# Performance work log

Measured on AMD Instinct MI355X. Metric: run time of the kernel, lower is better.

The kernel has to match this reference:

```python
import jax, jax.numpy as jnp
import numpy as np

NORMALIZE_EPS = 1e-5
INV_DELTA = 15.0
DIST_NORM_PREV = 0.5  # init value of _dist_norm_prev buffer (eval-mode constant)
SKIP_OFFSET = 2


def _l2_normalize(v, axis, eps=NORMALIZE_EPS):
    # matches torch F.normalize: v / max(||v||, eps)
    n = jnp.sqrt(jnp.sum(v * v, axis=axis, keepdims=True))
    return v / jnp.maximum(n, eps)


def setup_inputs() -> dict:
    key = jax.random.key(0)
    k1, k2 = jax.random.split(key)
    x = jax.random.normal(k1, (128, 197, 768), dtype=jnp.float32)
    emb = jnp.clip(jax.random.normal(k2, (4096, 768), dtype=jnp.float32), 0.0, None)
    emb = _l2_normalize(emb, axis=1)
    return {"x": x, "embedding": emb}


def reference(x, embedding):
    # drop CLS token -> [N, L, C] with L = H*W
    x = x[:, 1:, :]
    N, L, C = x.shape
    height = width = int(np.sqrt(L))
    # assign_words: L2-normalize tokens, cosine distance to codebook
    xn = _l2_normalize(x, axis=2)
    dist = -jnp.einsum("nlc,kc->nlk", xn, embedding)  # [N, L, K]
    inv_delta = INV_DELTA / DIST_NORM_PREV
    codes = jax.nn.softmax(-inv_delta * dist, axis=2)  # [N, L, K]
    # compute_bow: drop border tokens, mean-pool, L1-normalize
    grid = jnp.arange(height * width).reshape(height, width)
    keep = grid[SKIP_OFFSET:-SKIP_OFFSET, SKIP_OFFSET:-SKIP_OFFSET].reshape(-1)
    bow = jnp.mean(codes[:, keep, :], axis=1)  # [N, K]
    bow = bow / jnp.maximum(jnp.sum(jnp.abs(bow), axis=1, keepdims=True), NORMALIZE_EPS)
    return bow, codes
```

## Files before the change

### kernel.cpp

```cpp
#include <hip/hip_runtime.h>


typedef unsigned short ushort_t;
typedef short short8 __attribute__((ext_vector_type(8)));
typedef float float4_ __attribute__((ext_vector_type(4)));

#define M_ROWS 25088
#define N_COLS 4096
#define K_DIM  768
#define BM 128
#define BN 128
#define BK 32

__device__ __forceinline__ unsigned short f2bf_rne(float f) {
  unsigned u = __float_as_uint(f);
  unsigned r = u + 0x7fffu + ((u >> 16) & 1u);
  return (unsigned short)(r >> 16);
}
__device__ __forceinline__ float bf2f(unsigned short h) {
  return __uint_as_float(((unsigned)h) << 16);
}

__device__ __forceinline__ void gload16(const void* g, void* l) {
  __builtin_amdgcn_global_load_lds(
      (__attribute__((address_space(1))) void*)g,
      (__attribute__((address_space(3))) void*)l, 16, 0, 0);
}

__global__ void split_emb_kernel(const float* __restrict__ emb,
                                 ushort_t* __restrict__ Bh,
                                 ushort_t* __restrict__ Bl) {
  int t = blockIdx.x * 256 + threadIdx.x;
  float f = emb[t];
  unsigned short h = f2bf_rne(f);
  Bh[t] = h;
  Bl[t] = f2bf_rne(f - bf2f(h));
}

__global__ void norm_split_x_kernel(const float* __restrict__ x,
                                    ushort_t* __restrict__ Ah,
                                    ushort_t* __restrict__ Al) {
  int m = blockIdx.x;
  int n = m / 196;
  int l = m - n * 196;
  size_t src = ((size_t)n * 197 + 1 + l) * 768;
  int t = threadIdx.x;

  float v0 = x[src + t];
  float v1 = x[src + t + 256];
  float v2 = x[src + t + 512];
  float s = v0 * v0 + v1 * v1 + v2 * v2;
  #pragma unroll
  for (int off = 32; off; off >>= 1) s += __shfl_xor(s, off, 64);
  __shared__ float ws4[4];
  if ((t & 63) == 0) ws4[t >> 6] = s;
  __syncthreads();
  s = ws4[0] + ws4[1] + ws4[2] + ws4[3];
  float scale = 1.0f / fmaxf(sqrtf(s), 1e-5f);

  size_t dst = (size_t)m * 768;
  float f[3] = {v0 * scale, v1 * scale, v2 * scale};
  int idx[3] = {t, t + 256, t + 512};
  #pragma unroll
  for (int i = 0; i < 3; i++) {
    unsigned short h = f2bf_rne(f[i]);
    Ah[dst + idx[i]] = h;
    Al[dst + idx[i]] = f2bf_rne(f[i] - bf2f(h));
  }
}

__global__ __launch_bounds__(256, 2)
void gemm_exp_kernel(const ushort_t* __restrict__ Ah, const ushort_t* __restrict__ Al,
                     const ushort_t* __restrict__ Bh, const ushort_t* __restrict__ Bl,
                     float* __restrict__ codes, float* __restrict__ rowsum) {
  __shared__ __attribute__((aligned(16))) ushort_t sAh[BM * BK];
  __shared__ __attribute__((aligned(16))) ushort_t sAl[BM * BK];
  __shared__ __attribute__((aligned(16))) ushort_t sBh[BM * BK];
  __shared__ __attribute__((aligned(16))) ushort_t sBl[BM * BK];
  __shared__ float rs[BM];

  const int t = threadIdx.x;
  const int w = t >> 6;
  const int lane = t & 63;
  const int row0 = blockIdx.x * BM;
  const int col0 = blockIdx.y * BN;

  if (t < BM) rs[t] = 0.f;

  float4_ acc[4][4];
  #pragma unroll
  for (int i = 0; i < 4; i++)
    #pragma unroll
    for (int j = 0; j < 4; j++) acc[i][j] = (float4_){0.f, 0.f, 0.f, 0.f};

  const int r0 = t >> 2;
  const int c0 = (((t & 3) ^ ((r0 >> 1) & 3))) * 8;
  const ushort_t* gA = Ah + (size_t)(row0 + r0) * K_DIM + c0;
  const ushort_t* gAl_ = Al + (size_t)(row0 + r0) * K_DIM + c0;
  const ushort_t* gB = Bh + (size_t)(col0 + r0) * K_DIM + c0;
  const ushort_t* gBl_ = Bl + (size_t)(col0 + r0) * K_DIM + c0;
  const int half = 64 * K_DIM;
  const int ldsw = w * 512;

  const int rl = (w >> 1) * 64;
  const int cl = (w & 1) * 64;
  const int lq = lane >> 4;
  const int li = lane & 15;
  const int fsw = (li >> 1) & 3;
  const int abase = (rl + li) * BK + (lq ^ fsw) * 8;
  const int bbase = (cl + li) * BK + (lq ^ fsw) * 8;

  for (int kk = 0; kk < K_DIM; kk += BK) {
    __syncthreads();
    gload16(gA + kk,           sAh + ldsw);
    gload16(gA + kk + half,    sAh + 2048 + ldsw);
    gload16(gAl_ + kk,         sAl + ldsw);
    gload16(gAl_ + kk + half,  sAl + 2048 + ldsw);
    gload16(gB + kk,           sBh + ldsw);
    gload16(gB + kk + half,    sBh + 2048 + ldsw);
    gload16(gBl_ + kk,         sBl + ldsw);
    gload16(gBl_ + kk + half,  sBl + 2048 + ldsw);
    __syncthreads();

    short8 ah[4], al[4], bh[4], bl[4];
    #pragma unroll
    for (int i = 0; i < 4; i++) {
      ah[i] = *(const short8*)(sAh + abase + i * 16 * BK);
      al[i] = *(const short8*)(sAl + abase + i * 16 * BK);
      bh[i] = *(const short8*)(sBh + bbase + i * 16 * BK);
      bl[i] = *(const short8*)(sBl + bbase + i * 16 * BK);
    }
    #pragma unroll
    for (int i = 0; i < 4; i++)
      #pragma unroll
      for (int j = 0; j < 4; j++) {
        acc[i][j] = __builtin_amdgcn_mfma_f32_16x16x32_bf16(ah[i], bh[j], acc[i][j], 0, 0, 0);
        acc[i][j] = __builtin_amdgcn_mfma_f32_16x16x32_bf16(ah[i], bl[j], acc[i][j], 0, 0, 0);
        acc[i][j] = __builtin_amdgcn_mfma_f32_16x16x32_bf16(al[i], bh[j], acc[i][j], 0, 0, 0);
      }
  }

  float rsum[4][4];
  #pragma unroll
  for (int i = 0; i < 4; i++)
    #pragma unroll
    for (int r = 0; r < 4; r++) rsum[i][r] = 0.f;

  #pragma unroll
  for (int i = 0; i < 4; i++)
    #pragma unroll
    for (int j = 0; j < 4; j++)
      #pragma unroll
      for (int r = 0; r < 4; r++) {
        float e = __expf(30.0f * acc[i][j][r]);
        size_t row = (size_t)(row0 + rl + i * 16 + lq * 4 + r);
        size_t col = (size_t)(col0 + cl + j * 16 + li);
        codes[row * N_COLS + col] = e;
        rsum[i][r] += e;
      }

  #pragma unroll
  for (int i = 0; i < 4; i++)
    #pragma unroll
    for (int r = 0; r < 4; r++) {
      float v = rsum[i][r];
      v += __shfl_xor(v, 1, 64);
      v += __shfl_xor(v, 2, 64);
      v += __shfl_xor(v, 4, 64);
      v += __shfl_xor(v, 8, 64);
      if (li == 0) atomicAdd(&rs[rl + i * 16 + lq * 4 + r], v);
    }
  __syncthreads();
  if (t < BM) atomicAdd(&rowsum[row0 + t], rs[t]);
}

__global__ __launch_bounds__(256)
void rescale_bow_kernel(float* __restrict__ codes,
                        const float* __restrict__ rowsum,
                        float* __restrict__ bow_un,
                        float* __restrict__ bow_l1) {
  const int n = blockIdx.x >> 2;
  const int t = threadIdx.x;
  const int k4 = (blockIdx.x & 3) * 256 + t;

  __shared__ float inv[196];
  __shared__ float keep[196];
  if (t < 196) {
    inv[t] = 1.0f / rowsum[n * 196 + t];
    int rr = t / 14;
    int cc = t - rr * 14;
    keep[t] = (rr >= 2 && rr <= 11 && cc >= 2 && cc <= 11) ? 0.01f : 0.0f;
  }
  __syncthreads();

  float4_* base = (float4_*)(codes + (size_t)n * 196 * N_COLS) + k4;
  float4_ acc = {0.f, 0.f, 0.f, 0.f};
  #pragma unroll 2
  for (int l = 0; l < 196; l++) {
    float4_ v = base[(size_t)l * 1024];
    float iv = inv[l];
    v.x *= iv; v.y *= iv; v.z *= iv; v.w *= iv;
    base[(size_t)l * 1024] = v;
    float kf = keep[l];
    acc.x += kf * v.x; acc.y += kf * v.y;
    acc.z += kf * v.z; acc.w += kf * v.w;
  }

  ((float4_*)(bow_un + (size_t)n * N_COLS))[k4] = acc;

  float s = fabsf(acc.x) + fabsf(acc.y) + fabsf(acc.z) + fabsf(acc.w);
  #pragma unroll
  for (int off = 32; off; off >>= 1) s += __shfl_xor(s, off, 64);
  __shared__ float wsum[4];
  if ((t & 63) == 0) wsum[t >> 6] = s;
  __syncthreads();
  if (t == 0) atomicAdd(&bow_l1[n], wsum[0] + wsum[1] + wsum[2] + wsum[3]);
}

__global__ void bow_norm_kernel(const float* __restrict__ bow_un,
                                const float* __restrict__ bow_l1,
                                float* __restrict__ bow_out) {
  int t = blockIdx.x * 256 + threadIdx.x;
  int n = t >> 12;
  bow_out[t] = bow_un[t] / fmaxf(bow_l1[n], 1e-5f);
}

extern "C" void kernel_launch(void* const* d_in, const int* in_sizes, int n_in,
                              void* d_out, int out_size, void* d_ws, size_t ws_size,
                              hipStream_t stream) {
  const float* x = (const float*)d_in[0];
  const float* emb = (const float*)d_in[1];
  float* bow_out = (float*)d_out;
  float* codes = (float*)d_out + 524288;

  char* ws = (char*)d_ws;
  ushort_t* Ah = (ushort_t*)(ws + 0);
  ushort_t* Al = (ushort_t*)(ws + 38535168);
  ushort_t* Bh = (ushort_t*)(ws + 77070336);
  ushort_t* Bl = (ushort_t*)(ws + 83361792);
  float* rowsum = (float*)(ws + 89653248);
  float* bow_un = (float*)(ws + 89753600);
  float* bow_l1 = (float*)(ws + 91850752);

  hipMemsetAsync(rowsum, 0, 25088 * 4, stream);
  hipMemsetAsync(bow_l1, 0, 128 * 4, stream);

  split_emb_kernel<<<12288, 256, 0, stream>>>(emb, Bh, Bl);
  norm_split_x_kernel<<<25088, 256, 0, stream>>>(x, Ah, Al);

  dim3 ggrid(M_ROWS / BM, N_COLS / BN);
  gemm_exp_kernel<<<ggrid, 256, 0, stream>>>(Ah, Al, Bh, Bl, codes, rowsum);

  rescale_bow_kernel<<<512, 256, 0, stream>>>(codes, rowsum, bow_un, bow_l1);
  bow_norm_kernel<<<2048, 256, 0, stream>>>(bow_un, bow_l1, bow_out);
}
```

Measured before the change: 1.084 ms.

## Split rescale over token groups with atomics, fuse L1 norm, raise GEMM occupancy

The rescale/bow kernel now splits the 196 tokens of each image into 4 groups of 49, launching 2048 blocks instead of 512. Each block unrolls loads 7 at a time for more memory-level parallelism and accumulates partial bow sums with float atomics into a zeroed buffer. The L1 norm reduction moves into a per-image bow_norm kernel. Separately, the GEMM's launch bounds are raised to 4 waves-per-SIMD occupancy, which may force register spills given its large accumulator and fragment arrays.

```diff
diff --git a/kernel.cpp b/kernel.cpp
--- a/kernel.cpp
+++ b/kernel.cpp
@@ -69,7 +69,7 @@
   }
 }
 
-__global__ __launch_bounds__(256, 2)
+__global__ __launch_bounds__(256, 4)
 void gemm_exp_kernel(const ushort_t* __restrict__ Ah, const ushort_t* __restrict__ Al,
                      const ushort_t* __restrict__ Bh, const ushort_t* __restrict__ Bl,
                      float* __restrict__ codes, float* __restrict__ rowsum) {
@@ -177,52 +177,79 @@
 __global__ __launch_bounds__(256)
 void rescale_bow_kernel(float* __restrict__ codes,
                         const float* __restrict__ rowsum,
-                        float* __restrict__ bow_un,
-                        float* __restrict__ bow_l1) {
-  const int n = blockIdx.x >> 2;
+                        float* __restrict__ bow_un) {
+  const int bid = blockIdx.x;
+  const int n = bid >> 4;
+  const int g = (bid >> 2) & 3;
+  const int chunk = bid & 3;
   const int t = threadIdx.x;
-  const int k4 = (blockIdx.x & 3) * 256 + t;
-
-  __shared__ float inv[196];
-  __shared__ float keep[196];
-  if (t < 196) {
-    inv[t] = 1.0f / rowsum[n * 196 + t];
-    int rr = t / 14;
-    int cc = t - rr * 14;
+  const int k4 = chunk * 256 + t;
+  const int l0 = g * 49;
+
+  __shared__ float inv[49];
+  __shared__ float keep[49];
+  if (t < 49) {
+    int l = l0 + t;
+    inv[t] = 1.0f / rowsum[n * 196 + l];
+    int rr = l / 14;
+    int cc = l - rr * 14;
     keep[t] = (rr >= 2 && rr <= 11 && cc >= 2 && cc <= 11) ? 0.01f : 0.0f;
   }
   __syncthreads();
 
-  float4_* base = (float4_*)(codes + (size_t)n * 196 * N_COLS) + k4;
+  float4_* base = (float4_*)(codes + (size_t)n * 196 * N_COLS)
+                  + (size_t)l0 * 1024 + k4;
   float4_ acc = {0.f, 0.f, 0.f, 0.f};
-  #pragma unroll 2
-  for (int l = 0; l < 196; l++) {
-    float4_ v = base[(size_t)l * 1024];
-    float iv = inv[l];
-    v.x *= iv; v.y *= iv; v.z *= iv; v.w *= iv;
-    base[(size_t)l * 1024] = v;
-    float kf = keep[l];
-    acc.x += kf * v.x; acc.y += kf * v.y;
-    acc.z += kf * v.z; acc.w += kf * v.w;
-  }
-
-  ((float4_*)(bow_un + (size_t)n * N_COLS))[k4] = acc;
-
-  float s = fabsf(acc.x) + fabsf(acc.y) + fabsf(acc.z) + fabsf(acc.w);
+  #pragma unroll
+  for (int c = 0; c < 7; c++) {
+    float4_ v[7];
+    #pragma unroll
+    for (int u = 0; u < 7; u++) v[u] = base[(size_t)(c * 7 + u) * 1024];
+    #pragma unroll
+    for (int u = 0; u < 7; u++) {
+      int l = c * 7 + u;
+      float iv = inv[l];
+      v[u].x *= iv; v[u].y *= iv; v[u].z *= iv; v[u].w *= iv;
+      base[(size_t)l * 1024] = v[u];
+      float kf = keep[l];
+      acc.x += kf * v[u].x; acc.y += kf * v[u].y;
+      acc.z += kf * v[u].z; acc.w += kf * v[u].w;
+    }
+  }
+
+  float* dst = bow_un + (size_t)n * N_COLS + (size_t)k4 * 4;
+  atomicAdd(dst + 0, acc.x);
+  atomicAdd(dst + 1, acc.y);
+  atomicAdd(dst + 2, acc.z);
+  atomicAdd(dst + 3, acc.w);
+}
+
+__global__ __launch_bounds__(256)
+void bow_norm_kernel(const float* __restrict__ bow_un,
+                     float* __restrict__ bow_out) {
+  const int n = blockIdx.x;
+  const int t = threadIdx.x;
+  const float4_* src = (const float4_*)(bow_un + (size_t)n * N_COLS);
+  float4_ v[4];
+  float s = 0.f;
+  #pragma unroll
+  for (int i = 0; i < 4; i++) {
+    v[i] = src[t + i * 256];
+    s += fabsf(v[i].x) + fabsf(v[i].y) + fabsf(v[i].z) + fabsf(v[i].w);
+  }
   #pragma unroll
   for (int off = 32; off; off >>= 1) s += __shfl_xor(s, off, 64);
-  __shared__ float wsum[4];
-  if ((t & 63) == 0) wsum[t >> 6] = s;
-  __syncthreads();
-  if (t == 0) atomicAdd(&bow_l1[n], wsum[0] + wsum[1] + wsum[2] + wsum[3]);
-}
-
-__global__ void bow_norm_kernel(const float* __restrict__ bow_un,
-                                const float* __restrict__ bow_l1,
-                                float* __restrict__ bow_out) {
-  int t = blockIdx.x * 256 + threadIdx.x;
-  int n = t >> 12;
-  bow_out[t] = bow_un[t] / fmaxf(bow_l1[n], 1e-5f);
+  __shared__ float ws4[4];
+  if ((t & 63) == 0) ws4[t >> 6] = s;
+  __syncthreads();
+  float invn = 1.0f / fmaxf(ws4[0] + ws4[1] + ws4[2] + ws4[3], 1e-5f);
+  float4_* dst = (float4_*)(bow_out + (size_t)n * N_COLS);
+  #pragma unroll
+  for (int i = 0; i < 4; i++) {
+    float4_ o = v[i];
+    o.x *= invn; o.y *= invn; o.z *= invn; o.w *= invn;
+    dst[t + i * 256] = o;
+  }
 }
 
 extern "C" void kernel_launch(void* const* d_in, const int* in_sizes, int n_in,
@@ -240,10 +267,9 @@
   ushort_t* Bl = (ushort_t*)(ws + 83361792);
   float* rowsum = (float*)(ws + 89653248);
   float* bow_un = (float*)(ws + 89753600);
-  float* bow_l1 = (float*)(ws + 91850752);
 
   hipMemsetAsync(rowsum, 0, 25088 * 4, stream);
-  hipMemsetAsync(bow_l1, 0, 128 * 4, stream);
+  hipMemsetAsync(bow_un, 0, 524288 * 4, stream);
 
   split_emb_kernel<<<12288, 256, 0, stream>>>(emb, Bh, Bl);
   norm_split_x_kernel<<<25088, 256, 0, stream>>>(x, Ah, Al);
@@ -251,6 +277,6 @@
   dim3 ggrid(M_ROWS / BM, N_COLS / BN);
   gemm_exp_kernel<<<ggrid, 256, 0, stream>>>(Ah, Al, Bh, Bl, codes, rowsum);
 
-  rescale_bow_kernel<<<512, 256, 0, stream>>>(codes, rowsum, bow_un, bow_l1);
-  bow_norm_kernel<<<2048, 256, 0, stream>>>(bow_un, bow_l1, bow_out);
-}
+  rescale_bow_kernel<<<2048, 256, 0, stream>>>(codes, rowsum, bow_un);
+  bow_norm_kernel<<<128, 256, 0, stream>>>(bow_un, bow_out);
+}
```

Result: slower. 1.121 ms (+3.4%).
